# Kernel tuning notes

Hardware: AMD Instinct MI355X
Metric: run time of the kernel (lower is better)

Reference implementation:

```python
import jax, jax.numpy as jnp
import numpy as np

B, CIN, COUT, H, W = 16, 64, 64, 256, 256
MX, MY = 64, 64  # retained spectral modes (NxW, NyW)
NY_R = W // 2 + 1  # rfft length of last dim


def _dequant(q, scale, min_val):
    # matches torch: (q.float() + 127) * scale + min_val, q in [-127, 128]
    return (q.astype(jnp.float32) + 127.0) * scale + min_val


def setup_inputs() -> dict:
    key = jax.random.key(0)
    k0, k1, k2, k3 = jax.random.split(key, 4)
    x = jax.random.normal(k0, (B, CIN, H, W), dtype=jnp.float32)
    q_real = jax.random.randint(k1, (CIN, COUT, MX, MY), -127, 129, dtype=jnp.int32)
    q_imag = jax.random.randint(k2, (CIN, COUT, MX, MY), -127, 129, dtype=jnp.int32)
    q_bias = jax.random.randint(k3, (COUT,), -127, 129, dtype=jnp.int32)
    return {
        "x": x,
        "q_real": q_real,
        "q_imag": q_imag,
        "q_bias": q_bias,
        "scale_real": jnp.float32(2e-3),
        "min_real": jnp.float32(-0.25),
        "scale_imag": jnp.float32(2e-3),
        "min_imag": jnp.float32(-0.25),
        "b_scale": jnp.float32(1e-4),
        "b_min": jnp.float32(-0.0128),
    }


def reference(x, q_real, q_imag, q_bias, scale_real, min_real, scale_imag, min_imag, b_scale, b_min):
    # 1) rFFT over the last two (spatial) dims, norm='backward' (torch default)
    x_fft = jnp.fft.rfftn(x, axes=(-2, -1), norm="backward")  # [B, Cin, H, NY_R] complex

    # 2) inline dequantize the complex spectral weight
    w_real = _dequant(q_real, scale_real, min_real)
    w_imag = _dequant(q_imag, scale_imag, min_imag)
    Wc = jax.lax.complex(w_real, w_imag)  # [Cin, Cout, MX, MY]

    # 3) center slices as in the torch forward
    cx, nx = H // 2, MX // 2
    sx = slice(cx - nx, cx + (MX - nx))
    cy, ny = NY_R // 2, MY // 2
    sy = slice(cy - ny, cy + (MY - ny))

    # fused channel multiply-accumulate (replaces the nested python loop)
    out_slice = jnp.einsum("bixy,ioxy->boxy", x_fft[:, :, sx, sy], Wc)

    out_fft = jnp.zeros((B, COUT, H, NY_R), dtype=x_fft.dtype)
    out_fft = out_fft.at[:, :, sx, sy].set(out_slice)

    # 4) inverse rFFT back to spatial domain
    x_out = jnp.fft.irfftn(out_fft, s=(H, W), axes=(-2, -1), norm="backward")

    # 5) dequantized bias, broadcast over (1, Cout, 1, 1)
    bias = _dequant(q_bias, b_scale, b_min)
    return x_out + bias[None, :, None, None]
```

## Files before the change

### kernel.cpp

```cpp
#include <hip/hip_runtime.h>


#define HW    256
#define NCIN  64
#define NCOUT 64
#define NB    16
#define R0    96
#define C0    32

typedef __bf16 bf16x2 __attribute__((ext_vector_type(2)));
typedef __bf16 bf16x8 __attribute__((ext_vector_type(8)));
typedef float  f32x4  __attribute__((ext_vector_type(4)));

__device__ __forceinline__ unsigned short f2bf(float f) {
    __bf16 h = (__bf16)f;
    return __builtin_bit_cast(unsigned short, h);
}
__device__ __forceinline__ unsigned pk2(float a, float b) {
    bf16x2 v;
    v.x = (__bf16)a;
    v.y = (__bf16)b;
    return __builtin_bit_cast(unsigned, v);
}
__device__ __forceinline__ bf16x8 ld_frag_g(const unsigned short* p) {
    return __builtin_bit_cast(bf16x8, *(const uint4*)p);
}
__device__ __forceinline__ void gload_lds16(const unsigned short* g, unsigned short* l) {
    __builtin_amdgcn_global_load_lds(
        (const __attribute__((address_space(1))) unsigned int*)g,
        (__attribute__((address_space(3))) unsigned int*)l, 16, 0, 0);
}
__device__ __forceinline__ void gload_lds16f(const float* g, float* l) {
    __builtin_amdgcn_global_load_lds(
        (const __attribute__((address_space(1))) unsigned int*)g,
        (__attribute__((address_space(3))) unsigned int*)l, 16, 0, 0);
}

__global__ void build_all_tables(unsigned short* __restrict__ A1tab,
                                 unsigned short* __restrict__ B2T,
                                 unsigned short* __restrict__ B1fT,
                                 unsigned short* __restrict__ A2f) {
    int idx = blockIdx.x * 256 + threadIdx.x;
    const float TPO = 0.0245436926061702596754f;
    float s, c;
    if (idx < 32768) {
        int h = idx >> 7;
        int k = idx & 127;
        int kk = k & 63;
        __sincosf((float)(((R0 + kk) * h) & 255) * TPO, &s, &c);
        A1tab[idx] = f2bf(k < 64 ? c : s);
        __sincosf((float)(((C0 + kk) * h) & 255) * TPO, &s, &c);
        B2T[idx] = f2bf(k < 64 ? c : -s);
    } else if (idx < 65536) {
        int j = idx - 32768;
        int cc = j >> 8, w = j & 255;
        __sincosf((float)(((C0 + (cc & 63)) * w) & 255) * TPO, &s, &c);
        B1fT[(cc << 8) | (w ^ ((cc & 7) << 3))] = f2bf(cc < 64 ? c : -s);
    } else {
        int j = idx - 65536;
        int mr = j >> 9, k = j & 511;
        __sincosf((float)(((R0 + (mr & 63)) * (k & 255)) & 255) * TPO, &s, &c);
        float v = (mr < 64) ? ((k < 256) ? c : s)
                            : ((k < 256) ? -s : c);
        A2f[j] = f2bf(v);
    }
}

__global__ __launch_bounds__(512, 4) void fwd_mfma(
        const float*          __restrict__ x,
        const unsigned short* __restrict__ B1fT,
        const unsigned short* __restrict__ A2f,
        float*                __restrict__ Xout) {
    __shared__ __align__(16) unsigned short smem[32768];
    int bi = blockIdx.x;
    const float* xim = x + (size_t)bi * 65536;
    int t = threadIdx.x, lane = t & 63, wv = t >> 6;
    int g = lane >> 4, lr = lane & 15;

    #pragma unroll
    for (int i = 0; i < 8; ++i)
        gload_lds16(B1fT + i * 4096 + t * 8, &smem[i * 4096 + wv * 512]);

    const float* xrow[2];
    #pragma unroll
    for (int mf = 0; mf < 2; ++mf)
        xrow[mf] = xim + (wv * 32 + mf * 16 + lr) * 256 + g * 8;
    __syncthreads();

    f32x4 acc[2][8];
    #pragma unroll
    for (int mf = 0; mf < 2; ++mf)
        #pragma unroll
        for (int nf = 0; nf < 8; ++nf) acc[mf][nf] = (f32x4)0.0f;

    #pragma unroll
    for (int ks = 0; ks < 8; ++ks) {
        int k0 = ks * 32 + g * 8;
        bf16x8 a[2];
        #pragma unroll
        for (int mf = 0; mf < 2; ++mf) {
            float4 v0 = *(const float4*)(xrow[mf] + ks * 32);
            float4 v1 = *(const float4*)(xrow[mf] + ks * 32 + 4);
            uint4 pk;
            pk.x = pk2(v0.x, v0.y); pk.y = pk2(v0.z, v0.w);
            pk.z = pk2(v1.x, v1.y); pk.w = pk2(v1.z, v1.w);
            a[mf] = __builtin_bit_cast(bf16x8, pk);
        }
        #pragma unroll
        for (int half = 0; half < 2; ++half) {
            bf16x8 b[4];
            #pragma unroll
            for (int j = 0; j < 4; ++j) {
                int n = (half * 4 + j) * 16 + lr;
                b[j] = __builtin_bit_cast(bf16x8,
                         *(const uint4*)&smem[n * 256 + (k0 ^ ((n & 7) << 3))]);
            }
            #pragma unroll
            for (int mf = 0; mf < 2; ++mf)
                #pragma unroll
                for (int j = 0; j < 4; ++j)
                    acc[mf][half * 4 + j] = __builtin_amdgcn_mfma_f32_16x16x32_bf16(
                        a[mf], b[j], acc[mf][half * 4 + j], 0, 0, 0);
        }
    }
    __syncthreads();

    #pragma unroll
    for (int mf = 0; mf < 2; ++mf)
        #pragma unroll
        for (int nf = 0; nf < 8; ++nf) {
            int cl  = nf * 16 + lr;
            int col = cl & 63;
            int h0  = wv * 32 + mf * 16 + g * 4;
            int kk0 = (cl < 64) ? h0 : (256 + h0);
            uint2 pk;
            pk.x = pk2(acc[mf][nf][0], acc[mf][nf][1]);
            pk.y = pk2(acc[mf][nf][2], acc[mf][nf][3]);
            *(uint2*)&smem[col * 512 + (kk0 ^ ((col & 7) << 3))] = pk;
        }
    __syncthreads();

    f32x4 acc2[4];
    #pragma unroll
    for (int nf = 0; nf < 4; ++nf) acc2[nf] = (f32x4)0.0f;
    const unsigned short* a2row = A2f + (wv * 16 + lr) * 512;
    #pragma unroll
    for (int ks = 0; ks < 16; ++ks) {
        int k0 = ks * 32 + g * 8;
        bf16x8 a2 = ld_frag_g(a2row + k0);
        #pragma unroll
        for (int nf = 0; nf < 4; ++nf) {
            int c = nf * 16 + lr;
            bf16x8 b2 = __builtin_bit_cast(bf16x8,
                          *(const uint4*)&smem[c * 512 + (k0 ^ ((c & 7) << 3))]);
            acc2[nf] = __builtin_amdgcn_mfma_f32_16x16x32_bf16(a2, b2, acc2[nf], 0, 0, 0);
        }
    }
    {
        int bb = bi >> 6, ii = bi & 63;
        #pragma unroll
        for (int nf = 0; nf < 4; ++nf)
            #pragma unroll
            for (int rg = 0; rg < 4; ++rg) {
                int m = wv * 16 + g * 4 + rg;
                int c = nf * 16 + lr;
                int r = m & 63, p = m >> 6;
                Xout[(size_t)r * 131072 + ii * 2048 + bb * 128 + p * 64 + c]
                    = acc2[nf][rg];
            }
    }
}

__global__ __launch_bounds__(256) void mix_kernel(
        const float* __restrict__ X,
        const int*   __restrict__ q_real,
        const int*   __restrict__ q_imag,
        const float* __restrict__ s_r, const float* __restrict__ m_r,
        const float* __restrict__ s_i, const float* __restrict__ m_i,
        unsigned*    __restrict__ Yb) {
    int rr = blockIdx.x;
    int ot = blockIdx.y;
    int t  = threadIdx.x, lane = t & 63, wv = t >> 6;
    int cp = t & 31;
    int oq = t >> 5;
    int o  = ot * 8 + oq;
    int c0 = cp * 2;
    float sr = *s_r, mr = *m_r, si = *s_i, mi = *m_i;

    __shared__ __align__(16) float sh[2][2048];
    const float* xsl = X + (size_t)rr * 131072;

    const int* qrp = q_real + (size_t)o * 4096 + rr * 64 + c0;
    const int* qip = q_imag + (size_t)o * 4096 + rr * 64 + c0;

    float Yr0[16], Yi0[16], Yr1[16], Yi1[16];
    #pragma unroll
    for (int b = 0; b < 16; ++b) { Yr0[b] = 0.f; Yi0[b] = 0.f; Yr1[b] = 0.f; Yi1[b] = 0.f; }

    int2 wqr[2], wqi[2];
    wqr[0] = *(const int2*)(qrp);
    wqi[0] = *(const int2*)(qip);
    wqr[1] = *(const int2*)(qrp + 262144);
    wqi[1] = *(const int2*)(qip + 262144);
    {
        const float* src = xsl + wv * 512;
        gload_lds16f(src + lane * 4,       &sh[0][wv * 512]);
        gload_lds16f(src + 256 + lane * 4, &sh[0][wv * 512 + 256]);
    }
    __syncthreads();

    #pragma unroll 2
    for (int i = 0; i < 64; ++i) {
        const int cur = i & 1;
        if (i < 63) {
            const float* src = xsl + (i + 1) * 2048 + wv * 512;
            gload_lds16f(src + lane * 4,       &sh[cur ^ 1][wv * 512]);
            gload_lds16f(src + 256 + lane * 4, &sh[cur ^ 1][wv * 512 + 256]);
        }
        float wr0 = (float)(wqr[cur].x + 127) * sr + mr;
        float wr1 = (float)(wqr[cur].y + 127) * sr + mr;
        float wi0 = (float)(wqi[cur].x + 127) * si + mi;
        float wi1 = (float)(wqi[cur].y + 127) * si + mi;
        if (i < 62) {
            wqr[cur] = *(const int2*)(qrp + (size_t)(i + 2) * 262144);
            wqi[cur] = *(const int2*)(qip + (size_t)(i + 2) * 262144);
        }
        #pragma unroll
        for (int b = 0; b < 16; ++b) {
            float2 xr = *(const float2*)&sh[cur][b * 128 + c0];
            float2 xi = *(const float2*)&sh[cur][b * 128 + 64 + c0];
            Yr0[b] += xr.x * wr0 - xi.x * wi0;
            Yi0[b] += xr.x * wi0 + xi.x * wr0;
            Yr1[b] += xr.y * wr1 - xi.y * wi1;
            Yi1[b] += xr.y * wi1 + xi.y * wr1;
        }
        if (i < 63) __syncthreads();
    }

    #pragma unroll
    for (int b = 0; b < 16; ++b) {
        uint2 v;
        v.x = pk2(Yr0[b], Yi0[b]);
        v.y = pk2(Yr1[b], Yi1[b]);
        *(uint2*)&Yb[(size_t)(b * NCOUT + o) * 4096 + rr * 64 + c0] = v;
    }
}

__global__ __launch_bounds__(256, 2) void inv_mfma(
        const unsigned*       __restrict__ Y,
        const unsigned short* __restrict__ A1tab,
        const unsigned short* __restrict__ B2T,
        const int*            __restrict__ q_bias,
        const float* __restrict__ b_s, const float* __restrict__ b_m,
        float*                __restrict__ out) {
    __shared__ __align__(16) unsigned short smem[32768];
    int bo   = blockIdx.x;
    int t    = threadIdx.x;
    int lane = t & 63;
    int wv   = t >> 6;
    int g    = lane >> 4;
    int lr   = lane & 15;
    float bias = ((float)q_bias[bo & 63] + 127.0f) * (*b_s) + (*b_m);

    {
        const unsigned* Yp = Y + (size_t)bo * 4096;
        uint4 y0 = *(const uint4*)(Yp + t * 16);
        uint4 y1 = *(const uint4*)(Yp + t * 16 + 4);
        uint4 y2 = *(const uint4*)(Yp + t * 16 + 8);
        uint4 y3 = *(const uint4*)(Yp + t * 16 + 12);
        unsigned ys[16] = {y0.x, y0.y, y0.z, y0.w, y1.x, y1.y, y1.z, y1.w,
                           y2.x, y2.y, y2.z, y2.w, y3.x, y3.y, y3.z, y3.w};
        int r  = t >> 2;
        int cb = (t & 3) * 16;
        #pragma unroll
        for (int j = 0; j < 16; ++j) {
            int c = cb + j;
            unsigned y = ys[j];
            unsigned short yr  = (unsigned short)(y & 0xFFFFu);
            unsigned short yi  = (unsigned short)(y >> 16);
            unsigned short nyi = (unsigned short)(yi ^ 0x8000u);
            int sw = (c & 7) << 3;
            smem[c * 128        + ((r)      ^ sw)] = yr;
            smem[c * 128        + ((64 + r) ^ sw)] = nyi;
            smem[(64 + c) * 128 + ((r)      ^ sw)] = yi;
            smem[(64 + c) * 128 + ((64 + r) ^ sw)] = yr;
        }
    }
    __syncthreads();

    f32x4 acc[4][8];
    #pragma unroll
    for (int mf = 0; mf < 4; ++mf)
        #pragma unroll
        for (int nf = 0; nf < 8; ++nf) acc[mf][nf] = (f32x4)0.0f;

    #pragma unroll
    for (int ks = 0; ks < 4; ++ks) {
        int k0 = ks * 32 + g * 8;
        bf16x8 a[4], b[8];
        #pragma unroll
        for (int mf = 0; mf < 4; ++mf) {
            int h = wv * 64 + mf * 16 + lr;
            a[mf] = ld_frag_g(A1tab + h * 128 + k0);
        }
        #pragma unroll
        for (int nf = 0; nf < 8; ++nf) {
            int n = nf * 16 + lr;
            b[nf] = ld_frag_g(&smem[n * 128 + (k0 ^ ((n & 7) << 3))]);
        }
        #pragma unroll
        for (int mf = 0; mf < 4; ++mf)
            #pragma unroll
            for (int nf = 0; nf < 8; ++nf)
                acc[mf][nf] = __builtin_amdgcn_mfma_f32_16x16x32_bf16(
                                  a[mf], b[nf], acc[mf][nf], 0, 0, 0);
    }
    __syncthreads();

    #pragma unroll
    for (int mf = 0; mf < 4; ++mf)
        #pragma unroll
        for (int nf = 0; nf < 8; ++nf)
            #pragma unroll
            for (int rg = 0; rg < 4; ++rg) {
                int h = wv * 64 + mf * 16 + g * 4 + rg;
                int k = nf * 16 + lr;
                smem[h * 128 + (k ^ ((h & 7) << 3))] = f2bf(acc[mf][nf][rg]);
            }
    __syncthreads();

    const float scale = 2.0f / 65536.0f;
    float* outp = out + (size_t)bo * 65536;
    #pragma unroll
    for (int nh = 0; nh < 2; ++nh) {
        f32x4 acc2[4][8];
        #pragma unroll
        for (int mf = 0; mf < 4; ++mf)
            #pragma unroll
            for (int nf = 0; nf < 8; ++nf) acc2[mf][nf] = (f32x4)0.0f;

        #pragma unroll
        for (int ks = 0; ks < 4; ++ks) {
            int k0 = ks * 32 + g * 8;
            bf16x8 a[4], b[8];
            #pragma unroll
            for (int mf = 0; mf < 4; ++mf) {
                int h = wv * 64 + mf * 16 + lr;
                a[mf] = ld_frag_g(&smem[h * 128 + (k0 ^ ((h & 7) << 3))]);
            }
            #pragma unroll
            for (int nf = 0; nf < 8; ++nf) {
                int w = nh * 128 + nf * 16 + lr;
                b[nf] = ld_frag_g(B2T + w * 128 + k0);
            }
            #pragma unroll
            for (int mf = 0; mf < 4; ++mf)
                #pragma unroll
                for (int nf = 0; nf < 8; ++nf)
                    acc2[mf][nf] = __builtin_amdgcn_mfma_f32_16x16x32_bf16(
                                       a[mf], b[nf], acc2[mf][nf], 0, 0, 0);
        }
        #pragma unroll
        for (int mf = 0; mf < 4; ++mf)
            #pragma unroll
            for (int rg = 0; rg < 4; ++rg) {
                int h = wv * 64 + mf * 16 + g * 4 + rg;
                float* row = outp + h * 256 + nh * 128 + lr;
                #pragma unroll
                for (int nf = 0; nf < 8; ++nf)
                    row[nf * 16] = acc2[mf][nf][rg] * scale + bias;
            }
    }
}

extern "C" void kernel_launch(void* const* d_in, const int* in_sizes, int n_in,
                              void* d_out, int out_size, void* d_ws, size_t ws_size,
                              hipStream_t stream) {
    const float* x          = (const float*)d_in[0];
    const int*   q_real     = (const int*)  d_in[1];
    const int*   q_imag     = (const int*)  d_in[2];
    const int*   q_bias     = (const int*)  d_in[3];
    const float* scale_real = (const float*)d_in[4];
    const float* min_real   = (const float*)d_in[5];
    const float* scale_imag = (const float*)d_in[6];
    const float* min_imag   = (const float*)d_in[7];
    const float* b_scale    = (const float*)d_in[8];
    const float* b_min      = (const float*)d_in[9];
    float* out = (float*)d_out;

    float* ws = (float*)d_ws;
    unsigned short* A1tab = (unsigned short*)(ws);
    unsigned short* B2T   = (unsigned short*)(ws + 16384);
    unsigned short* B1fT  = (unsigned short*)(ws + 32768);
    unsigned short* A2f   = (unsigned short*)(ws + 49152);
    float*          Xws   = (float*)   (ws + 81920);
    unsigned*       Ybws  = (unsigned*)(ws + 81920 + 8388608);

    build_all_tables<<<512, 256, 0, stream>>>(A1tab, B2T, B1fT, A2f);
    fwd_mfma<<<NB * NCIN, 512, 0, stream>>>(x, B1fT, A2f, Xws);
    mix_kernel<<<dim3(64, 8), 256, 0, stream>>>(Xws, q_real, q_imag,
                                                scale_real, min_real,
                                                scale_imag, min_imag, Ybws);
    inv_mfma<<<NB * NCOUT, 256, 0, stream>>>(Ybws, A1tab, B2T,
                                             q_bias, b_scale, b_min, out);
}
```

Baseline: 273.7 us.

## Stream input image through double-buffered LDS and read DFT twiddles from global

The forward kernel now stages the fp32 input rows into LDS in 32-column chunks with async global-to-LDS loads, double buffered and paced by explicit vmcnt waits, so loads overlap the MFMA work. The twiddle table B1fT, which was previously staged in LDS, is now read directly from global/L2 per fragment, and its swizzle is dropped from the table layout. This cuts the upfront twiddle staging and synchronisation but adds repeated global loads of the twiddle matrix inside the inner loop. It also relies on the hand-written waitcnt sequencing being correct, since no barrier separates chunks.

```diff
diff --git a/kernel.cpp b/kernel.cpp
--- a/kernel.cpp
+++ b/kernel.cpp
@@ -55,7 +55,7 @@
         int j = idx - 32768;
         int cc = j >> 8, w = j & 255;
         __sincosf((float)(((C0 + (cc & 63)) * w) & 255) * TPO, &s, &c);
-        B1fT[(cc << 8) | (w ^ ((cc & 7) << 3))] = f2bf(cc < 64 ? c : -s);
+        B1fT[j] = f2bf(cc < 64 ? c : -s);
     } else {
         int j = idx - 65536;
         int mr = j >> 9, k = j & 511;
@@ -71,49 +71,62 @@
         const unsigned short* __restrict__ B1fT,
         const unsigned short* __restrict__ A2f,
         float*                __restrict__ Xout) {
-    __shared__ __align__(16) unsigned short smem[32768];
+    __shared__ __align__(16) float smemF[16384];
     int bi = blockIdx.x;
     const float* xim = x + (size_t)bi * 65536;
     int t = threadIdx.x, lane = t & 63, wv = t >> 6;
     int g = lane >> 4, lr = lane & 15;
 
-    #pragma unroll
-    for (int i = 0; i < 8; ++i)
-        gload_lds16(B1fT + i * 4096 + t * 8, &smem[i * 4096 + wv * 512]);
-
-    const float* xrow[2];
+    const int rhi = lane >> 3;
+    const int cg  = (lane & 7) ^ rhi;
+    const float* xsrc0 = xim + (wv * 32 + rhi) * 256 + cg * 4;
+
+#define ISSUE_CHUNK(chn, bufF)                                         \
+    {   const float* s_ = xsrc0 + (chn) * 32;                          \
+        float*       d_ = (bufF) + wv * 1024;                          \
+        gload_lds16f(s_,            d_);                               \
+        gload_lds16f(s_ + 2048,     d_ + 256);                         \
+        gload_lds16f(s_ + 4096,     d_ + 512);                         \
+        gload_lds16f(s_ + 6144,     d_ + 768);  }
+
+    float* buf0 = smemF;
+    float* buf1 = smemF + 8192;
+    ISSUE_CHUNK(0, buf0);
+
+    f32x4 acc[2][8];
     #pragma unroll
     for (int mf = 0; mf < 2; ++mf)
-        xrow[mf] = xim + (wv * 32 + mf * 16 + lr) * 256 + g * 8;
-    __syncthreads();
-
-    f32x4 acc[2][8];
-    #pragma unroll
-    for (int mf = 0; mf < 2; ++mf)
         #pragma unroll
         for (int nf = 0; nf < 8; ++nf) acc[mf][nf] = (f32x4)0.0f;
 
     #pragma unroll
-    for (int ks = 0; ks < 8; ++ks) {
-        int k0 = ks * 32 + g * 8;
+    for (int ch = 0; ch < 8; ++ch) {
+        float* xb = (ch & 1) ? buf1 : buf0;
+        if (ch < 7) ISSUE_CHUNK(ch + 1, (ch & 1) ? buf0 : buf1);
+        if (ch < 7) asm volatile("s_waitcnt vmcnt(4)" ::: "memory");
+        else        asm volatile("s_waitcnt vmcnt(0)" ::: "memory");
+        __builtin_amdgcn_sched_barrier(0);
+
         bf16x8 a[2];
         #pragma unroll
         for (int mf = 0; mf < 2; ++mf) {
-            float4 v0 = *(const float4*)(xrow[mf] + ks * 32);
-            float4 v1 = *(const float4*)(xrow[mf] + ks * 32 + 4);
+            int rl = mf * 16 + lr;
+            const float* rp = xb + wv * 1024 + rl * 32;
+            float4 p0 = *(const float4*)(rp + (((2 * g)     ^ (rl & 7)) * 4));
+            float4 p1 = *(const float4*)(rp + (((2 * g + 1) ^ (rl & 7)) * 4));
             uint4 pk;
-            pk.x = pk2(v0.x, v0.y); pk.y = pk2(v0.z, v0.w);
-            pk.z = pk2(v1.x, v1.y); pk.w = pk2(v1.z, v1.w);
+            pk.x = pk2(p0.x, p0.y); pk.y = pk2(p0.z, p0.w);
+            pk.z = pk2(p1.x, p1.y); pk.w = pk2(p1.z, p1.w);
             a[mf] = __builtin_bit_cast(bf16x8, pk);
         }
+        int k0 = ch * 32 + g * 8;
         #pragma unroll
         for (int half = 0; half < 2; ++half) {
             bf16x8 b[4];
             #pragma unroll
             for (int j = 0; j < 4; ++j) {
                 int n = (half * 4 + j) * 16 + lr;
-                b[j] = __builtin_bit_cast(bf16x8,
-                         *(const uint4*)&smem[n * 256 + (k0 ^ ((n & 7) << 3))]);
+                b[j] = ld_frag_g(B1fT + n * 256 + k0);
             }
             #pragma unroll
             for (int mf = 0; mf < 2; ++mf)
@@ -123,8 +136,10 @@
                         a[mf], b[j], acc[mf][half * 4 + j], 0, 0, 0);
         }
     }
-    __syncthreads();
-
+#undef ISSUE_CHUNK
+    __syncthreads();
+
+    unsigned short* bop = (unsigned short*)smemF;
     #pragma unroll
     for (int mf = 0; mf < 2; ++mf)
         #pragma unroll
@@ -136,7 +151,7 @@
             uint2 pk;
             pk.x = pk2(acc[mf][nf][0], acc[mf][nf][1]);
             pk.y = pk2(acc[mf][nf][2], acc[mf][nf][3]);
-            *(uint2*)&smem[col * 512 + (kk0 ^ ((col & 7) << 3))] = pk;
+            *(uint2*)&bop[col * 512 + (kk0 ^ ((col & 7) << 3))] = pk;
         }
     __syncthreads();
 
@@ -152,7 +167,7 @@
         for (int nf = 0; nf < 4; ++nf) {
             int c = nf * 16 + lr;
             bf16x8 b2 = __builtin_bit_cast(bf16x8,
-                          *(const uint4*)&smem[c * 512 + (k0 ^ ((c & 7) << 3))]);
+                          *(const uint4*)&bop[c * 512 + (k0 ^ ((c & 7) << 3))]);
             acc2[nf] = __builtin_amdgcn_mfma_f32_16x16x32_bf16(a2, b2, acc2[nf], 0, 0, 0);
         }
     }
```

New measurement: 290.1 us. 6.0% more time.
